# Kernel optimization log

Measured on AMD Instinct MI355X. Metric: run time of the kernel, lower is better.

Reference implementation:

```python
import jax, jax.numpy as jnp
import numpy as np

N = 50000      # nodes
E = 800000     # edges (before self loops)
D = 128        # embedding_dimension
HEADS = 4
C = 32         # hidden_channels
NEG_SLOPE = 0.2


def setup_inputs() -> dict:
    key = jax.random.key(0)
    ks = jax.random.split(key, 12)
    s = 0.1
    x = jax.random.normal(ks[0], (N, D), jnp.float32)
    edge_index = jax.random.randint(ks[1], (2, E), 0, N)
    # layer 1: D -> HEADS*C, concat
    W1 = jax.random.normal(ks[2], (D, HEADS * C), jnp.float32) * s
    a_src1 = jax.random.normal(ks[3], (HEADS, C), jnp.float32) * s
    a_dst1 = jax.random.normal(ks[4], (HEADS, C), jnp.float32) * s
    b1 = jnp.zeros((HEADS * C,), jnp.float32)
    # layer 2: HEADS*C -> HEADS*C, concat
    W2 = jax.random.normal(ks[5], (HEADS * C, HEADS * C), jnp.float32) * s
    a_src2 = jax.random.normal(ks[6], (HEADS, C), jnp.float32) * s
    a_dst2 = jax.random.normal(ks[7], (HEADS, C), jnp.float32) * s
    b2 = jnp.zeros((HEADS * C,), jnp.float32)
    # layer 3: HEADS*C -> C, heads=1, no concat (mean over the single head)
    W3 = jax.random.normal(ks[8], (HEADS * C, C), jnp.float32) * s
    a_src3 = jax.random.normal(ks[9], (1, C), jnp.float32) * s
    a_dst3 = jax.random.normal(ks[10], (1, C), jnp.float32) * s
    b3 = jnp.zeros((C,), jnp.float32)
    return {"x": x, "edge_index": edge_index,
            "W1": W1, "a_src1": a_src1, "a_dst1": a_dst1, "b1": b1,
            "W2": W2, "a_src2": a_src2, "a_dst2": a_dst2, "b2": b2,
            "W3": W3, "a_src3": a_src3, "a_dst3": a_dst3, "b3": b3}


def gat_layer(x, src, dst, W, a_s, a_d, b, heads, concat):
    """One PyG-style GATConv (eval mode: dropout inactive).
    x: [N, Fin]; src/dst: [E2] (self loops included)."""
    n = x.shape[0]
    h = (x @ W).reshape(n, heads, -1)                 # [N, H, C]
    alpha_src = (h * a_s).sum(-1)                     # [N, H]
    alpha_dst = (h * a_d).sum(-1)                     # [N, H]
    logits = jax.nn.leaky_relu(alpha_src[src] + alpha_dst[dst], NEG_SLOPE)  # [E2, H]
    # segment softmax over destination nodes
    m = jax.ops.segment_max(logits, dst, num_segments=n)          # [N, H]
    ex = jnp.exp(logits - m[dst])                                  # [E2, H]
    denom = jax.ops.segment_sum(ex, dst, num_segments=n)          # [N, H]
    alpha = ex / (denom[dst] + 1e-16)                              # [E2, H]
    msg = h[src] * alpha[:, :, None]                               # [E2, H, C]
    out = jax.ops.segment_sum(msg, dst, num_segments=n)            # [N, H, C]
    if concat:
        return out.reshape(n, -1) + b
    return out.mean(axis=1) + b


def reference(x, edge_index, W1, a_src1, a_dst1, b1, W2, a_src2, a_dst2, b2,
              W3, a_src3, a_dst3, b3):
    loops = jnp.arange(N, dtype=edge_index.dtype)
    src = jnp.concatenate([edge_index[0], loops])   # add_self_loops=True
    dst = jnp.concatenate([edge_index[1], loops])
    h = gat_layer(x, src, dst, W1, a_src1, a_dst1, b1, HEADS, True)
    h = jax.nn.elu(h)
    h = gat_layer(h, src, dst, W2, a_src2, a_dst2, b2, HEADS, True)
    h = jax.nn.elu(h)
    out = gat_layer(h, src, dst, W3, a_src3, a_dst3, b3, 1, False)
    return out
```

## Files before the change

kernel.cpp:

```cpp
#include <hip/hip_runtime.h>
#include <cmath>

constexpr int NN  = 50000;
constexpr int EE  = 800000;
constexpr int E2C = EE + NN;

constexpr int NBUCK = 256;
constexpr int BW    = 196;
constexpr int EPT   = 8;
constexpr int CH    = 256 * EPT;
constexpr int NB_B  = (E2C + CH - 1) / CH;
constexpr int CAP   = 4096;
constexpr int SCAP  = 5120;

using bf16x8 = __attribute__((ext_vector_type(8))) short;
using f32x4  = __attribute__((ext_vector_type(4))) float;

__device__ inline unsigned bf16rne(float f) {
    unsigned u = __builtin_bit_cast(unsigned, f);
    return (u + 0x7fffu + ((u >> 16) & 1u)) >> 16;
}
__device__ inline float bflo(unsigned u) { return __builtin_bit_cast(float, u << 16); }
__device__ inline float bfhi(unsigned u) { return __builtin_bit_cast(float, u & 0xffff0000u); }

__global__ __launch_bounds__(256) void cvt_weights(
    const float* __restrict__ W1, const float* __restrict__ W2,
    const float* __restrict__ W3,
    unsigned short* __restrict__ W1t, unsigned short* __restrict__ W2t,
    unsigned short* __restrict__ W3t, int* __restrict__ bcursor)
{
    int g = blockIdx.x * 256 + threadIdx.x;
    if (g < NBUCK) bcursor[g] = 0;
    const float* W; unsigned short* Wt; int cols;
    if (g < 2048)      { W = W1; Wt = W1t; cols = 128; }
    else if (g < 4096) { W = W2; Wt = W2t; cols = 128; g -= 2048; }
    else if (g < 4608) { W = W3; Wt = W3t; cols = 32;  g -= 4096; }
    else return;
    int c  = g / 16;
    int k8 = (g % 16) * 8;
    unsigned up[4];
    #pragma unroll
    for (int j = 0; j < 4; ++j) {
        float a = W[(k8 + 2 * j) * cols + c];
        float b = W[(k8 + 2 * j + 1) * cols + c];
        up[j] = bf16rne(a) | (bf16rne(b) << 16);
    }
    uint4 u; u.x = up[0]; u.y = up[1]; u.z = up[2]; u.w = up[3];
    *(uint4*)(Wt + c * 128 + k8) = u;
}

template<int NT, int NH, bool F32IN>
__device__ inline void gemm_body(
    int bid, const void* __restrict__ inv, const unsigned short* __restrict__ Wt,
    const float* __restrict__ a_s, const float* __restrict__ a_d,
    unsigned short* __restrict__ hout, float* __restrict__ asrc,
    float* __restrict__ adst)
{
    constexpr int COLS = NT * 16;
    constexpr int TPH  = NT / NH;
    const int lane = threadIdx.x & 63;
    const int wave = threadIdx.x >> 6;
    const int m    = lane & 15;
    const int quad = lane >> 4;
    const int n0   = bid * 64 + wave * 16;

    int arow = n0 + m; if (arow >= NN) arow = NN - 1;

    f32x4 acc[NT] = {};
    #pragma unroll
    for (int kq = 0; kq < 4; ++kq) {
        bf16x8 a;
        if constexpr (F32IN) {
            const float* ap = (const float*)inv + (long long)arow * 128 + quad * 8 + kq * 32;
            float4 v0 = *(const float4*)ap;
            float4 v1 = *(const float4*)(ap + 4);
            a[0] = (short)bf16rne(v0.x); a[1] = (short)bf16rne(v0.y);
            a[2] = (short)bf16rne(v0.z); a[3] = (short)bf16rne(v0.w);
            a[4] = (short)bf16rne(v1.x); a[5] = (short)bf16rne(v1.y);
            a[6] = (short)bf16rne(v1.z); a[7] = (short)bf16rne(v1.w);
        } else {
            a = *(const bf16x8*)((const unsigned short*)inv
                    + (long long)arow * 128 + quad * 8 + kq * 32);
        }
        #pragma unroll
        for (int t = 0; t < NT; ++t) {
            bf16x8 b = *(const bf16x8*)(Wt + (t * 16 + m) * 128 + kq * 32 + quad * 8);
            acc[t] = __builtin_amdgcn_mfma_f32_16x16x32_bf16(a, b, acc[t], 0, 0, 0);
        }
    }

    #pragma unroll
    for (int r = 0; r < 4; ++r) {
        int node = n0 + quad * 4 + r;
        if (node < NN) {
            #pragma unroll
            for (int t = 0; t < NT; ++t)
                hout[(long long)node * COLS + t * 16 + m] =
                    (unsigned short)bf16rne(acc[t][r]);
        }
    }

    float asv[NT], adv[NT];
    #pragma unroll
    for (int t = 0; t < NT; ++t) { asv[t] = a_s[t * 16 + m]; adv[t] = a_d[t * 16 + m]; }

    #pragma unroll
    for (int r = 0; r < 4; ++r) {
        const int node = n0 + quad * 4 + r;
        #pragma unroll
        for (int hh = 0; hh < NH; ++hh) {
            float ps = 0.f, pd = 0.f;
            #pragma unroll
            for (int q = 0; q < TPH; ++q) {
                int t = hh * TPH + q;
                ps = fmaf(acc[t][r], asv[t], ps);
                pd = fmaf(acc[t][r], adv[t], pd);
            }
            #pragma unroll
            for (int off = 8; off > 0; off >>= 1) {
                ps += __shfl_down(ps, off, 16);
                pd += __shfl_down(pd, off, 16);
            }
            if (m == 0 && node < NN) {
                asrc[node * NH + hh] = ps;
                adst[node * NH + hh] = pd;
            }
        }
    }

    if (bid == 0 && threadIdx.x == 0) {
        #pragma unroll
        for (int hh = 0; hh < NH; ++hh) asrc[NN * NH + hh] = -1e30f;
    }
}

template<int NT, int NH, bool F32IN>
__global__ __launch_bounds__(256) void gemm_mfma(
    const void* __restrict__ inv, const unsigned short* __restrict__ Wt,
    const float* __restrict__ a_s, const float* __restrict__ a_d,
    unsigned short* __restrict__ hout, float* __restrict__ asrc,
    float* __restrict__ adst)
{
    gemm_body<NT, NH, F32IN>(blockIdx.x, inv, Wt, a_s, a_d, hout, asrc, adst);
}

__global__ __launch_bounds__(256) void bucket_bin(
    const int* __restrict__ ei, int* __restrict__ bcursor,
    unsigned* __restrict__ pairs)
{
    __shared__ int cnt[NBUCK];
    __shared__ int scanex[NBUCK];
    __shared__ int base[NBUCK];
    __shared__ int cur[NBUCK];
    __shared__ unsigned stage[CH];

    const int tid = threadIdx.x;
    const long long e0 = (long long)blockIdx.x * CH;
    cnt[tid] = 0;
    __syncthreads();

    unsigned rec[EPT]; int bk[EPT];
    #pragma unroll
    for (int j = 0; j < EPT; ++j) {
        long long e = e0 + tid + j * 256;
        bool valid = e < E2C;
        int ss = 0, dd = 0;
        if (valid) {
            if (e < EE) { ss = ei[e]; dd = ei[EE + e]; }
            else        { ss = dd = (int)(e - EE); }
        }
        int b = dd / BW;
        bk[j]  = valid ? b : -1;
        rec[j] = (unsigned)ss | ((unsigned)(dd - b * BW) << 16) | ((unsigned)b << 24);
        if (valid) atomicAdd(&cnt[b], 1);
    }
    __syncthreads();

    const int myc = cnt[tid];
    scanex[tid] = myc;
    __syncthreads();
    for (int off = 1; off < NBUCK; off <<= 1) {
        int t = (tid >= off) ? scanex[tid - off] : 0;
        __syncthreads();
        scanex[tid] += t;
        __syncthreads();
    }
    int excl = scanex[tid] - myc;
    __syncthreads();
    scanex[tid] = excl;
    cur[tid]    = excl;
    base[tid]   = atomicAdd(&bcursor[tid], myc);
    __syncthreads();

    #pragma unroll
    for (int j = 0; j < EPT; ++j) {
        if (bk[j] >= 0) {
            int p = atomicAdd(&cur[bk[j]], 1);
            stage[p] = rec[j];
        }
    }
    __syncthreads();

    const int total = (e0 + CH <= E2C) ? CH : (int)(E2C - e0);
    for (int j = tid; j < total; j += 256) {
        unsigned p = stage[j];
        int b = (int)(p >> 24);
        pairs[(size_t)b * CAP + base[b] + (j - scanex[b])] = p;
    }
}

__device__ inline void sort_body(
    int b, const int* __restrict__ bcursor, const unsigned* __restrict__ pairs,
    int2* __restrict__ rowp, unsigned short* __restrict__ sorted_src)
{
    __shared__ int deg[256];
    __shared__ int scn[256];
    __shared__ int cur[256];
    const int n0 = b * BW;
    const int n1 = (n0 + BW < NN) ? n0 + BW : NN;
    const int nloc = n1 - n0;
    const int tid = threadIdx.x;
    const int mycnt = bcursor[b];
    const unsigned* seg = pairs + (size_t)b * CAP;
    const int base = b * SCAP;

    deg[tid] = 0;
    __syncthreads();
    for (int i = tid; i < mycnt; i += 256)
        atomicAdd(&deg[(seg[i] >> 16) & 0xff], 1);
    __syncthreads();

    const int pv = (deg[tid] + 3) & ~3;
    scn[tid] = pv;
    __syncthreads();
    for (int off = 1; off < 256; off <<= 1) {
        int t = (tid >= off) ? scn[tid - off] : 0;
        __syncthreads();
        scn[tid] += t;
        __syncthreads();
    }
    const int totalp = scn[255];
    const int pexcl  = scn[tid] - pv;
    cur[tid] = base + pexcl;
    if (tid < nloc) rowp[n0 + tid] = make_int2(base + pexcl, base + pexcl + pv);
    __syncthreads();

    int lim = totalp + 8; if (lim > SCAP) lim = SCAP;
    for (int i = tid; i < lim; i += 256)
        sorted_src[base + i] = (unsigned short)NN;
    if (b == NBUCK - 1 && tid < 8)
        sorted_src[NBUCK * SCAP + tid] = (unsigned short)NN;
    __syncthreads();
    for (int i = tid; i < mycnt; i += 256) {
        unsigned p = seg[i];
        int pos = atomicAdd(&cur[(p >> 16) & 0xff], 1);
        sorted_src[pos] = (unsigned short)(p & 0xffff);
    }
}

template<int NT, int NH, bool F32IN>
__global__ __launch_bounds__(256) void sort_gemm(
    const int* __restrict__ bcursor, const unsigned* __restrict__ pairs,
    int2* __restrict__ rowp, unsigned short* __restrict__ sorted_src,
    const void* __restrict__ inv, const unsigned short* __restrict__ Wt,
    const float* __restrict__ a_s, const float* __restrict__ a_d,
    unsigned short* __restrict__ hout, float* __restrict__ asrc,
    float* __restrict__ adst)
{
    if (blockIdx.x < NBUCK)
        sort_body(blockIdx.x, bcursor, pairs, rowp, sorted_src);
    else
        gemm_body<NT, NH, F32IN>(blockIdx.x - NBUCK, inv, Wt, a_s, a_d,
                                 hout, asrc, adst);
}

template<int COLS, int NH, bool DO_ELU, bool OUTBF>
__global__ __launch_bounds__(256) void aggr_csr(
    const int2* __restrict__ rowp, const unsigned short* __restrict__ sorted_src,
    const unsigned short* __restrict__ hin,
    const float* __restrict__ asrc, const float* __restrict__ adst,
    const float* __restrict__ bias, void* __restrict__ outv)
{
    constexpr int TPN = COLS / 8;
    constexpr int USTR = COLS / 2;
    int t = blockIdx.x * 256 + threadIdx.x;
    int d = t / TPN;
    int lc = t % TPN;
    if (d >= NN) return;
    const int cc = lc * 8;
    const int head = cc / 32;
    const float ad = adst[d * NH + head];
    const int2 be = rowp[d];
    const int beg = be.x, end = be.y;
    const uint* hp = (const uint*)hin + cc / 2;

    float num[8] = {};
    float den = 0.f;

    ushort4 sv = *(const ushort4*)&sorted_src[beg];
    for (int i = beg; i < end; i += 4) {
        ushort4 nx = *(const ushort4*)&sorted_src[i + 4];
        const int s[4] = {sv.x, sv.y, sv.z, sv.w};
        float a[4];
        uint4 Hv[4];
        #pragma unroll
        for (int j = 0; j < 4; ++j) a[j] = asrc[s[j] * NH + head];
        #pragma unroll
        for (int j = 0; j < 4; ++j)
            Hv[j] = *(const uint4*)&hp[(long long)s[j] * USTR];
        #pragma unroll
        for (int j = 0; j < 4; ++j) {
            float l = a[j] + ad; l = l > 0.f ? l : 0.2f * l;
            float w = __builtin_expf(l);
            den += w;
            num[0] = fmaf(w, bflo(Hv[j].x), num[0]); num[1] = fmaf(w, bfhi(Hv[j].x), num[1]);
            num[2] = fmaf(w, bflo(Hv[j].y), num[2]); num[3] = fmaf(w, bfhi(Hv[j].y), num[3]);
            num[4] = fmaf(w, bflo(Hv[j].z), num[4]); num[5] = fmaf(w, bfhi(Hv[j].z), num[5]);
            num[6] = fmaf(w, bflo(Hv[j].w), num[6]); num[7] = fmaf(w, bfhi(Hv[j].w), num[7]);
        }
        sv = nx;
    }

    float inv = 1.f / (den + 1e-16f);
    float v[8];
    #pragma unroll
    for (int j = 0; j < 8; ++j) {
        v[j] = num[j] * inv + bias[cc + j];
        if (DO_ELU) v[j] = v[j] > 0.f ? v[j] : expm1f(v[j]);
    }
    if constexpr (OUTBF) {
        uint4 u;
        u.x = bf16rne(v[0]) | (bf16rne(v[1]) << 16);
        u.y = bf16rne(v[2]) | (bf16rne(v[3]) << 16);
        u.z = bf16rne(v[4]) | (bf16rne(v[5]) << 16);
        u.w = bf16rne(v[6]) | (bf16rne(v[7]) << 16);
        *(uint4*)((unsigned short*)outv + (long long)d * COLS + cc) = u;
    } else {
        float4 o0 = {v[0], v[1], v[2], v[3]};
        float4 o1 = {v[4], v[5], v[6], v[7]};
        float* out = (float*)outv;
        *(float4*)&out[(long long)d * COLS + cc]     = o0;
        *(float4*)&out[(long long)d * COLS + cc + 4] = o1;
    }
}

extern "C" void kernel_launch(void* const* d_in, const int* in_sizes, int n_in,
                              void* d_out, int out_size, void* d_ws, size_t ws_size,
                              hipStream_t stream)
{
    const float* x   = (const float*)d_in[0];
    const int*   ei  = (const int*)  d_in[1];
    const float* W1  = (const float*)d_in[2];
    const float* as1 = (const float*)d_in[3];
    const float* ad1 = (const float*)d_in[4];
    const float* b1  = (const float*)d_in[5];
    const float* W2  = (const float*)d_in[6];
    const float* as2 = (const float*)d_in[7];
    const float* ad2 = (const float*)d_in[8];
    const float* b2  = (const float*)d_in[9];
    const float* W3  = (const float*)d_in[10];
    const float* as3 = (const float*)d_in[11];
    const float* ad3 = (const float*)d_in[12];
    const float* b3  = (const float*)d_in[13];
    float* out = (float*)d_out;

    unsigned short* H16 = (unsigned short*)d_ws;
    unsigned short* O16 = H16 + (size_t)(NN + 1) * 128;
    unsigned short* P16 = O16 + (size_t)NN * 128;
    unsigned short* W1t = P16 + (size_t)NN * 128;
    unsigned short* W2t = W1t + 128 * 128;
    unsigned short* W3t = W2t + 128 * 128;
    float* ASRC = (float*)(W3t + 32 * 128);
    float* ADST = ASRC + (size_t)(NN + 1) * 4;
    int2* rowp  = (int2*)(ADST + (size_t)NN * 4);
    unsigned short* sorted = (unsigned short*)(rowp + NN);
    int* bcursor = (int*)(sorted + (size_t)NBUCK * SCAP + 8);
    size_t off = ((size_t)(bcursor + NBUCK) - (size_t)d_ws + 15) & ~(size_t)15;
    unsigned* pairs = (unsigned*)((char*)d_ws + off);

    const int gCvtW    = (4608 + 255) / 256;
    const int gGemm    = (NN + 63) / 64;
    const int gSortG   = NBUCK + gGemm;
    const int gAggr128 = (NN * 16 + 255) / 256;
    const int gAggr32  = (NN * 4 + 255) / 256;

    cvt_weights<<<gCvtW, 256, 0, stream>>>(W1, W2, W3, W1t, W2t, W3t, bcursor);
    bucket_bin<<<NB_B, 256, 0, stream>>>(ei, bcursor, pairs);

    sort_gemm<8, 4, true><<<gSortG, 256, 0, stream>>>(
        bcursor, pairs, rowp, sorted, x, W1t, as1, ad1, H16, ASRC, ADST);
    aggr_csr<128, 4, true, true><<<gAggr128, 256, 0, stream>>>(
        rowp, sorted, H16, ASRC, ADST, b1, O16);

    gemm_mfma<8, 4, false><<<gGemm, 256, 0, stream>>>(O16, W2t, as2, ad2, H16, ASRC, ADST);
    aggr_csr<128, 4, true, true><<<gAggr128, 256, 0, stream>>>(
        rowp, sorted, H16, ASRC, ADST, b2, P16);

    gemm_mfma<2, 1, false><<<gGemm, 256, 0, stream>>>(P16, W3t, as3, ad3, H16, ASRC, ADST);
    aggr_csr<32, 1, false, false><<<gAggr32, 256, 0, stream>>>(
        rowp, sorted, H16, ASRC, ADST, b3, out);
}
```

Before: 271.6 us.

## Fuse aggregation with next-layer GEMM and split layer-1 GEMM across bin/sort kernels

Layers 1 and 2 now run their neighbour aggregation and the next layer's MFMA projection in one kernel. Each block aggregates 16 nodes into a swizzled LDS tile and then multiplies it by the next weight matrix, so the intermediate activations never round-trip through global memory and two launches disappear. The layer-1 GEMM blocks are also split between the bucket-binning launch and the sort launch to overlap work. Sentinel and padding initialisation moves into the weight-conversion kernel, and separate per-layer buffers replace the shared ones. The fused kernel has less parallelism in its GEMM phase, and for the 32-column output only one wave is active, which may leave the aggregation's latency less well hidden.

```diff
diff --git a/kernel.cpp b/kernel.cpp
--- a/kernel.cpp
+++ b/kernel.cpp
@@ -12,6 +12,8 @@
 constexpr int NB_B  = (E2C + CH - 1) / CH;
 constexpr int CAP   = 4096;
 constexpr int SCAP  = 5120;
+constexpr int G1ALL = (NN + 63) / 64;
+constexpr int G1A   = 391;
 
 using bf16x8 = __attribute__((ext_vector_type(8))) short;
 using f32x4  = __attribute__((ext_vector_type(4))) float;
@@ -27,10 +29,18 @@
     const float* __restrict__ W1, const float* __restrict__ W2,
     const float* __restrict__ W3,
     unsigned short* __restrict__ W1t, unsigned short* __restrict__ W2t,
-    unsigned short* __restrict__ W3t, int* __restrict__ bcursor)
+    unsigned short* __restrict__ W3t, int* __restrict__ bcursor,
+    float* __restrict__ AS1, float* __restrict__ AS2, float* __restrict__ AS3,
+    unsigned short* __restrict__ H1, unsigned short* __restrict__ H2,
+    unsigned short* __restrict__ H3)
 {
     int g = blockIdx.x * 256 + threadIdx.x;
     if (g < NBUCK) bcursor[g] = 0;
+    if (g < 4) { AS1[NN * 4 + g] = -1e30f; AS2[NN * 4 + g] = -1e30f; }
+    if (g == 4) AS3[NN] = -1e30f;
+    if (g < 128) { H1[(size_t)NN * 128 + g] = 0; H2[(size_t)NN * 128 + g] = 0; }
+    if (g < 32)  H3[(size_t)NN * 32 + g] = 0;
+
     const float* W; unsigned short* Wt; int cols;
     if (g < 2048)      { W = W1; Wt = W1t; cols = 128; }
     else if (g < 4096) { W = W2; Wt = W2t; cols = 128; g -= 2048; }
@@ -127,25 +137,10 @@
             }
         }
     }
-
-    if (bid == 0 && threadIdx.x == 0) {
-        #pragma unroll
-        for (int hh = 0; hh < NH; ++hh) asrc[NN * NH + hh] = -1e30f;
-    }
-}
-
-template<int NT, int NH, bool F32IN>
-__global__ __launch_bounds__(256) void gemm_mfma(
-    const void* __restrict__ inv, const unsigned short* __restrict__ Wt,
-    const float* __restrict__ a_s, const float* __restrict__ a_d,
-    unsigned short* __restrict__ hout, float* __restrict__ asrc,
-    float* __restrict__ adst)
-{
-    gemm_body<NT, NH, F32IN>(blockIdx.x, inv, Wt, a_s, a_d, hout, asrc, adst);
-}
-
-__global__ __launch_bounds__(256) void bucket_bin(
-    const int* __restrict__ ei, int* __restrict__ bcursor,
+}
+
+__device__ inline void bin_body(
+    int bid, const int* __restrict__ ei, int* __restrict__ bcursor,
     unsigned* __restrict__ pairs)
 {
     __shared__ int cnt[NBUCK];
@@ -155,7 +150,7 @@
     __shared__ unsigned stage[CH];
 
     const int tid = threadIdx.x;
-    const long long e0 = (long long)blockIdx.x * CH;
+    const long long e0 = (long long)bid * CH;
     cnt[tid] = 0;
     __syncthreads();
 
@@ -258,11 +253,24 @@
     }
 }
 
-template<int NT, int NH, bool F32IN>
+__global__ __launch_bounds__(256) void bin_gemm(
+    const int* __restrict__ ei, int* __restrict__ bcursor,
+    unsigned* __restrict__ pairs,
+    const float* __restrict__ x, const unsigned short* __restrict__ Wt,
+    const float* __restrict__ a_s, const float* __restrict__ a_d,
+    unsigned short* __restrict__ hout, float* __restrict__ asrc,
+    float* __restrict__ adst)
+{
+    if (blockIdx.x < NB_B)
+        bin_body(blockIdx.x, ei, bcursor, pairs);
+    else
+        gemm_body<8, 4, true>(blockIdx.x - NB_B, x, Wt, a_s, a_d, hout, asrc, adst);
+}
+
 __global__ __launch_bounds__(256) void sort_gemm(
     const int* __restrict__ bcursor, const unsigned* __restrict__ pairs,
     int2* __restrict__ rowp, unsigned short* __restrict__ sorted_src,
-    const void* __restrict__ inv, const unsigned short* __restrict__ Wt,
+    const float* __restrict__ x, const unsigned short* __restrict__ Wt,
     const float* __restrict__ a_s, const float* __restrict__ a_d,
     unsigned short* __restrict__ hout, float* __restrict__ asrc,
     float* __restrict__ adst)
@@ -270,23 +278,19 @@
     if (blockIdx.x < NBUCK)
         sort_body(blockIdx.x, bcursor, pairs, rowp, sorted_src);
     else
-        gemm_body<NT, NH, F32IN>(blockIdx.x - NBUCK, inv, Wt, a_s, a_d,
-                                 hout, asrc, adst);
-}
-
-template<int COLS, int NH, bool DO_ELU, bool OUTBF>
-__global__ __launch_bounds__(256) void aggr_csr(
+        gemm_body<8, 4, true>(blockIdx.x - NBUCK + G1A, x, Wt, a_s, a_d,
+                              hout, asrc, adst);
+}
+
+template<int COLS, int NH, bool DO_ELU>
+__device__ inline void aggr_node(
+    int d, int lc,
     const int2* __restrict__ rowp, const unsigned short* __restrict__ sorted_src,
     const unsigned short* __restrict__ hin,
     const float* __restrict__ asrc, const float* __restrict__ adst,
-    const float* __restrict__ bias, void* __restrict__ outv)
-{
-    constexpr int TPN = COLS / 8;
+    const float* __restrict__ bias, float v[8])
+{
     constexpr int USTR = COLS / 2;
-    int t = blockIdx.x * 256 + threadIdx.x;
-    int d = t / TPN;
-    int lc = t % TPN;
-    if (d >= NN) return;
     const int cc = lc * 8;
     const int head = cc / 32;
     const float ad = adst[d * NH + head];
@@ -322,26 +326,114 @@
     }
 
     float inv = 1.f / (den + 1e-16f);
-    float v[8];
     #pragma unroll
     for (int j = 0; j < 8; ++j) {
         v[j] = num[j] * inv + bias[cc + j];
         if (DO_ELU) v[j] = v[j] > 0.f ? v[j] : expm1f(v[j]);
     }
-    if constexpr (OUTBF) {
-        uint4 u;
-        u.x = bf16rne(v[0]) | (bf16rne(v[1]) << 16);
-        u.y = bf16rne(v[2]) | (bf16rne(v[3]) << 16);
-        u.z = bf16rne(v[4]) | (bf16rne(v[5]) << 16);
-        u.w = bf16rne(v[6]) | (bf16rne(v[7]) << 16);
-        *(uint4*)((unsigned short*)outv + (long long)d * COLS + cc) = u;
-    } else {
-        float4 o0 = {v[0], v[1], v[2], v[3]};
-        float4 o1 = {v[4], v[5], v[6], v[7]};
-        float* out = (float*)outv;
-        *(float4*)&out[(long long)d * COLS + cc]     = o0;
-        *(float4*)&out[(long long)d * COLS + cc + 4] = o1;
-    }
+}
+
+template<int NT_OUT, int NH_OUT>
+__global__ __launch_bounds__(256) void aggr_gemm(
+    const int2* __restrict__ rowp, const unsigned short* __restrict__ sorted_src,
+    const unsigned short* __restrict__ hin,
+    const float* __restrict__ asrc_in, const float* __restrict__ adst_in,
+    const float* __restrict__ bias,
+    const unsigned short* __restrict__ Wt,
+    const float* __restrict__ a_s, const float* __restrict__ a_d,
+    unsigned short* __restrict__ hout, float* __restrict__ asrc_out,
+    float* __restrict__ adst_out)
+{
+    __shared__ unsigned short lds_h[16 * 128];
+    const int tid = threadIdx.x;
+    const int row = tid / 16;
+    const int lc  = tid % 16;
+    const int d   = blockIdx.x * 16 + row;
+
+    float v[8];
+    aggr_node<128, 4, true>(d, lc, rowp, sorted_src, hin, asrc_in, adst_in,
+                            bias, v);
+
+    uint4 u;
+    u.x = bf16rne(v[0]) | (bf16rne(v[1]) << 16);
+    u.y = bf16rne(v[2]) | (bf16rne(v[3]) << 16);
+    u.z = bf16rne(v[4]) | (bf16rne(v[5]) << 16);
+    u.w = bf16rne(v[6]) | (bf16rne(v[7]) << 16);
+    *(uint4*)((char*)lds_h + row * 256 + ((lc * 16) ^ ((row & 7) << 4))) = u;
+    __syncthreads();
+
+    const int lane = tid & 63;
+    const int wave = tid >> 6;
+    const int m    = lane & 15;
+    const int quad = lane >> 4;
+    int t0;
+    if constexpr (NT_OUT == 8) t0 = wave * 2;
+    else { if (wave != 0) return; t0 = 0; }
+
+    f32x4 acc[2] = {};
+    #pragma unroll
+    for (int kq = 0; kq < 4; ++kq) {
+        int colb = (quad * 16 + kq * 64) ^ ((m & 7) << 4);
+        bf16x8 a = *(const bf16x8*)((const char*)lds_h + m * 256 + colb);
+        #pragma unroll
+        for (int tt = 0; tt < 2; ++tt) {
+            bf16x8 b = *(const bf16x8*)(Wt + ((t0 + tt) * 16 + m) * 128
+                                        + kq * 32 + quad * 8);
+            acc[tt] = __builtin_amdgcn_mfma_f32_16x16x32_bf16(a, b, acc[tt], 0, 0, 0);
+        }
+    }
+
+    constexpr int COLS_OUT = NT_OUT * 16;
+    const int head = t0 / (NT_OUT / NH_OUT);
+    const int n0   = blockIdx.x * 16;
+    float asv[2], adv[2];
+    #pragma unroll
+    for (int tt = 0; tt < 2; ++tt) {
+        asv[tt] = a_s[(t0 + tt) * 16 + m];
+        adv[tt] = a_d[(t0 + tt) * 16 + m];
+    }
+
+    #pragma unroll
+    for (int r = 0; r < 4; ++r) {
+        const int node = n0 + quad * 4 + r;
+        #pragma unroll
+        for (int tt = 0; tt < 2; ++tt)
+            hout[(long long)node * COLS_OUT + (t0 + tt) * 16 + m] =
+                (unsigned short)bf16rne(acc[tt][r]);
+        float ps = acc[0][r] * asv[0];
+        ps = fmaf(acc[1][r], asv[1], ps);
+        float pd = acc[0][r] * adv[0];
+        pd = fmaf(acc[1][r], adv[1], pd);
+        #pragma unroll
+        for (int off = 8; off > 0; off >>= 1) {
+            ps += __shfl_down(ps, off, 16);
+            pd += __shfl_down(pd, off, 16);
+        }
+        if (m == 0) {
+            asrc_out[node * NH_OUT + head] = ps;
+            adst_out[node * NH_OUT + head] = pd;
+        }
+    }
+}
+
+template<int COLS, int NH>
+__global__ __launch_bounds__(256) void aggr_final(
+    const int2* __restrict__ rowp, const unsigned short* __restrict__ sorted_src,
+    const unsigned short* __restrict__ hin,
+    const float* __restrict__ asrc, const float* __restrict__ adst,
+    const float* __restrict__ bias, float* __restrict__ out)
+{
+    constexpr int TPN = COLS / 8;
+    int t = blockIdx.x * 256 + threadIdx.x;
+    int d = t / TPN;
+    int lc = t % TPN;
+    if (d >= NN) return;
+    float v[8];
+    aggr_node<COLS, NH, false>(d, lc, rowp, sorted_src, hin, asrc, adst, bias, v);
+    float4 o0 = {v[0], v[1], v[2], v[3]};
+    float4 o1 = {v[4], v[5], v[6], v[7]};
+    *(float4*)&out[(long long)d * COLS + lc * 8]     = o0;
+    *(float4*)&out[(long long)d * COLS + lc * 8 + 4] = o1;
 }
 
 extern "C" void kernel_launch(void* const* d_in, const int* in_sizes, int n_in,
@@ -364,39 +456,40 @@
     const float* b3  = (const float*)d_in[13];
     float* out = (float*)d_out;
 
-    unsigned short* H16 = (unsigned short*)d_ws;
-    unsigned short* O16 = H16 + (size_t)(NN + 1) * 128;
-    unsigned short* P16 = O16 + (size_t)NN * 128;
-    unsigned short* W1t = P16 + (size_t)NN * 128;
+    unsigned short* H1  = (unsigned short*)d_ws;
+    unsigned short* H2  = H1 + (size_t)(NN + 1) * 128;
+    unsigned short* H3  = H2 + (size_t)(NN + 1) * 128;
+    unsigned short* W1t = H3 + (size_t)(NN + 1) * 32;
     unsigned short* W2t = W1t + 128 * 128;
     unsigned short* W3t = W2t + 128 * 128;
-    float* ASRC = (float*)(W3t + 32 * 128);
-    float* ADST = ASRC + (size_t)(NN + 1) * 4;
-    int2* rowp  = (int2*)(ADST + (size_t)NN * 4);
+    float* AS1 = (float*)(W3t + 32 * 128);
+    float* AD1 = AS1 + (size_t)(NN + 1) * 4;
+    float* AS2 = AD1 + (size_t)NN * 4;
+    float* AD2 = AS2 + (size_t)(NN + 1) * 4;
+    float* AS3 = AD2 + (size_t)NN * 4;
+    float* AD3 = AS3 + (size_t)(NN + 1);
+    int2* rowp = (int2*)(AD3 + NN);
     unsigned short* sorted = (unsigned short*)(rowp + NN);
     int* bcursor = (int*)(sorted + (size_t)NBUCK * SCAP + 8);
     size_t off = ((size_t)(bcursor + NBUCK) - (size_t)d_ws + 15) & ~(size_t)15;
     unsigned* pairs = (unsigned*)((char*)d_ws + off);
 
-    const int gCvtW    = (4608 + 255) / 256;
-    const int gGemm    = (NN + 63) / 64;
-    const int gSortG   = NBUCK + gGemm;
-    const int gAggr128 = (NN * 16 + 255) / 256;
-    const int gAggr32  = (NN * 4 + 255) / 256;
-
-    cvt_weights<<<gCvtW, 256, 0, stream>>>(W1, W2, W3, W1t, W2t, W3t, bcursor);
-    bucket_bin<<<NB_B, 256, 0, stream>>>(ei, bcursor, pairs);
-
-    sort_gemm<8, 4, true><<<gSortG, 256, 0, stream>>>(
-        bcursor, pairs, rowp, sorted, x, W1t, as1, ad1, H16, ASRC, ADST);
-    aggr_csr<128, 4, true, true><<<gAggr128, 256, 0, stream>>>(
-        rowp, sorted, H16, ASRC, ADST, b1, O16);
-
-    gemm_mfma<8, 4, false><<<gGemm, 256, 0, stream>>>(O16, W2t, as2, ad2, H16, ASRC, ADST);
-    aggr_csr<128, 4, true, true><<<gAggr128, 256, 0, stream>>>(
-        rowp, sorted, H16, ASRC, ADST, b2, P16);
-
-    gemm_mfma<2, 1, false><<<gGemm, 256, 0, stream>>>(P16, W3t, as3, ad3, H16, ASRC, ADST);
-    aggr_csr<32, 1, false, false><<<gAggr32, 256, 0, stream>>>(
-        rowp, sorted, H16, ASRC, ADST, b3, out);
-}
+    const int gCvtW  = (4608 + 255) / 256;
+    const int gBinG  = NB_B + G1A;
+    const int gSortG = NBUCK + (G1ALL - G1A);
+    const int gFused = NN / 16;
+    const int gAggr3 = (NN * 4 + 255) / 256;
+
+    cvt_weights<<<gCvtW, 256, 0, stream>>>(W1, W2, W3, W1t, W2t, W3t, bcursor,
+                                           AS1, AS2, AS3, H1, H2, H3);
+    bin_gemm<<<gBinG, 256, 0, stream>>>(ei, bcursor, pairs,
+                                        x, W1t, as1, ad1, H1, AS1, AD1);
+    sort_gemm<<<gSortG, 256, 0, stream>>>(bcursor, pairs, rowp, sorted,
+                                          x, W1t, as1, ad1, H1, AS1, AD1);
+    aggr_gemm<8, 4><<<gFused, 256, 0, stream>>>(
+        rowp, sorted, H1, AS1, AD1, b1, W2t, as2, ad2, H2, AS2, AD2);
+    aggr_gemm<2, 1><<<gFused, 256, 0, stream>>>(
+        rowp, sorted, H2, AS2, AD2, b2, W3t, as3, ad3, H3, AS3, AD3);
+    aggr_final<32, 1><<<gAggr3, 256, 0, stream>>>(
+        rowp, sorted, H3, AS3, AD3, b3, out);
+}
```

Result: faster. 258.5 us (-4.8%).
